# Kernel tuning notes

Measured on AMD Instinct MI355X. Metric: run time of the kernel, lower is better.

## Reference

```python
import jax, jax.numpy as jnp
import numpy as np

D_IN = 4096
D_OUT = 4096
EPS_NORM = 1e-6
EPS_Q = 1e-8


def _ternary_quantize(w):
    # per-output-channel absmean scale, then round/clamp to {-1,0,1}
    gamma = jnp.mean(jnp.abs(w), axis=-1)
    w_q = jnp.clip(jnp.round(w / (gamma[:, None] + EPS_Q)), -1.0, 1.0)
    return w_q, gamma


def setup_inputs() -> dict:
    key = jax.random.key(0)
    kx, kw = jax.random.split(key)
    x = jax.random.normal(kx, (2, 4096, D_IN), dtype=jnp.float32)
    # kaiming-uniform-like init then ternarize (mirrors torch __init__)
    bound = 1.0 / np.sqrt(D_IN)
    w_init = jax.random.uniform(kw, (D_OUT, D_IN), minval=-bound, maxval=bound, dtype=jnp.float32)
    w_q, gamma = _ternary_quantize(w_init)
    norm_weight = jnp.ones((D_IN,), dtype=jnp.float32)
    return {"x": x, "norm_weight": norm_weight, "w_q": w_q, "gamma": gamma}


def reference(x, norm_weight, w_q, gamma):
    # RMSNorm
    rms = jnp.sqrt(jnp.mean(x * x, axis=-1, keepdims=True) + EPS_NORM)
    xn = x / rms * norm_weight
    # ternary linear (dense fp32 GEMM, math identical to F.linear) + per-channel scale
    y = jnp.einsum('bsd,od->bso', xn, w_q) * gamma
    return y
```

## Files before the change

kernel.cpp:

```cpp
#include <hip/hip_runtime.h>
#include <hip/hip_bf16.h>
#include <stdint.h>

#define D_IN  4096
#define D_OUT 4096
#define MROWS 8192

using i32x4 = __attribute__((ext_vector_type(4))) int;

__global__ __launch_bounds__(256) void prep_kernel(
    const float* __restrict__ x, const float* __restrict__ nw,
    signed char* __restrict__ xq, float* __restrict__ srow,
    const float* __restrict__ wq, signed char* __restrict__ wb) {
  const int b = blockIdx.x;
  const int t = threadIdx.x;

  if (b < MROWS) {
    const float4* xr  = (const float4*)(x + (size_t)b * D_IN);
    const float4* nw4 = (const float4*)nw;

    float4 p[4];
    float ss = 0.f, mx = 0.f;
#pragma unroll
    for (int i = 0; i < 4; ++i) {
      const float4 v = xr[i * 256 + t];
      const float4 w = nw4[i * 256 + t];
      ss += v.x * v.x + v.y * v.y + v.z * v.z + v.w * v.w;
      p[i].x = v.x * w.x; p[i].y = v.y * w.y;
      p[i].z = v.z * w.z; p[i].w = v.w * w.w;
      mx = fmaxf(mx, fmaxf(fmaxf(fabsf(p[i].x), fabsf(p[i].y)),
                           fmaxf(fabsf(p[i].z), fabsf(p[i].w))));
    }
#pragma unroll
    for (int off = 32; off > 0; off >>= 1) {
      ss += __shfl_down(ss, off, 64);
      mx = fmaxf(mx, __shfl_down(mx, off, 64));
    }

    __shared__ float rs[4], rm[4];
    if ((t & 63) == 0) { rs[t >> 6] = ss; rm[t >> 6] = mx; }
    __syncthreads();
    const float scale =
        rsqrtf((rs[0] + rs[1] + rs[2] + rs[3]) * (1.0f / D_IN) + 1e-6f);
    const float rowmax = fmaxf(fmaxf(rm[0], rm[1]), fmaxf(rm[2], rm[3])) * scale;
    const float s   = fmaxf(rowmax, 1e-20f) * (1.0f / 127.0f);
    const float f   = scale / s;
    if (t == 0) srow[b] = s;

    int* out = (int*)(xq + (size_t)b * D_IN);
#pragma unroll
    for (int i = 0; i < 4; ++i) {
      const int q0 = (int)rintf(p[i].x * f);
      const int q1 = (int)rintf(p[i].y * f);
      const int q2 = (int)rintf(p[i].z * f);
      const int q3 = (int)rintf(p[i].w * f);
      out[i * 256 + t] =
          (q0 & 0xFF) | ((q1 & 0xFF) << 8) | ((q2 & 0xFF) << 16) | (q3 << 24);
    }
  } else {
    const int cb = b - MROWS;
    const float4* w4 = (const float4*)wq;
    int* o = (int*)wb;
#pragma unroll
    for (int i = 0; i < 4; ++i) {
      const int idx = cb * 1024 + i * 256 + t;
      const float4 v = w4[idx];
      const int q0 = (int)v.x, q1 = (int)v.y, q2 = (int)v.z, q3 = (int)v.w;
      o[idx] = (q0 & 0xFF) | ((q1 & 0xFF) << 8) | ((q2 & 0xFF) << 16) | (q3 << 24);
    }
  }
}

#define BM 128
#define BN 128
#define BKB 64

__global__ __launch_bounds__(256) void gemm_kernel(
    const signed char* __restrict__ A,
    const signed char* __restrict__ B,
    const float* __restrict__ srow,
    const float* __restrict__ gamma,
    float* __restrict__ C) {
  __shared__ __align__(16) signed char sA[BM * BKB];
  __shared__ __align__(16) signed char sB[BN * BKB];

  const int tid  = threadIdx.x;
  const int lane = tid & 63;
  const int wv   = tid >> 6;
  const int wm   = wv & 1;
  const int wn   = wv >> 1;
  const int bn   = blockIdx.x;
  const int bm   = blockIdx.y;

  i32x4 acc[4][4];
#pragma unroll
  for (int i = 0; i < 4; ++i)
#pragma unroll
    for (int j = 0; j < 4; ++j) acc[i][j] = (i32x4){0, 0, 0, 0};

  const size_t aBase = (size_t)(bm * BM) * D_IN;
  const size_t bBase = (size_t)(bn * BN) * D_IN;

  int r_[2], cc_[2];
#pragma unroll
  for (int i = 0; i < 2; ++i) {
    const int c = i * 256 + tid;
    r_[i]  = c >> 2;
    cc_[i] = ((c & 3) ^ ((r_[i] >> 1) & 3)) * 16;
  }

  for (int k0 = 0; k0 < D_IN; k0 += BKB) {
#pragma unroll
    for (int i = 0; i < 2; ++i) {
      __builtin_amdgcn_global_load_lds(
          (__attribute__((address_space(1))) void*)(A + aBase + (size_t)r_[i] * D_IN + k0 + cc_[i]),
          (__attribute__((address_space(3))) void*)&sA[(i * 256 + wv * 64) * 16],
          16, 0, 0);
    }
#pragma unroll
    for (int i = 0; i < 2; ++i) {
      __builtin_amdgcn_global_load_lds(
          (__attribute__((address_space(1))) void*)(B + bBase + (size_t)r_[i] * D_IN + k0 + cc_[i]),
          (__attribute__((address_space(3))) void*)&sB[(i * 256 + wv * 64) * 16],
          16, 0, 0);
    }
    __syncthreads();

    i32x4 af[4], bfr[4];
    const int m0 = wm * 64 + (lane & 15);
    const int n0 = wn * 64 + (lane & 15);
    const int kk = (((lane >> 4) ^ ((lane >> 1) & 3))) * 16;
#pragma unroll
    for (int i = 0; i < 4; ++i) af[i]  = *(const i32x4*)&sA[(m0 + i * 16) * BKB + kk];
#pragma unroll
    for (int j = 0; j < 4; ++j) bfr[j] = *(const i32x4*)&sB[(n0 + j * 16) * BKB + kk];

#pragma unroll
    for (int i = 0; i < 4; ++i)
#pragma unroll
      for (int j = 0; j < 4; ++j)
        acc[i][j] = __builtin_amdgcn_mfma_i32_16x16x64_i8(af[i], bfr[j], acc[i][j], 0, 0, 0);

    __syncthreads();
  }

  const int col0 = bn * BN + wn * 64 + (lane & 15);
  const int row0 = bm * BM + wm * 64 + ((lane >> 4) * 4);
  float sr[4][4];
#pragma unroll
  for (int i = 0; i < 4; ++i)
#pragma unroll
    for (int r = 0; r < 4; ++r) sr[i][r] = srow[row0 + i * 16 + r];

#pragma unroll
  for (int j = 0; j < 4; ++j) {
    const float g = gamma[col0 + j * 16];
#pragma unroll
    for (int i = 0; i < 4; ++i) {
      const int rb = row0 + i * 16;
#pragma unroll
      for (int r = 0; r < 4; ++r) {
        C[(size_t)(rb + r) * D_OUT + (col0 + j * 16)] =
            (float)acc[i][j][r] * sr[i][r] * g;
      }
    }
  }
}

extern "C" void kernel_launch(void* const* d_in, const int* in_sizes, int n_in,
                              void* d_out, int out_size, void* d_ws, size_t ws_size,
                              hipStream_t stream) {
  const float* x     = (const float*)d_in[0];
  const float* nw    = (const float*)d_in[1];
  const float* wq    = (const float*)d_in[2];
  const float* gamma = (const float*)d_in[3];
  float* y = (float*)d_out;

  signed char* xq = (signed char*)d_ws;
  signed char* wb = xq + (size_t)MROWS * D_IN;
  float* srow = (float*)(wb + (size_t)D_OUT * D_IN);

  prep_kernel<<<MROWS + 4096, 256, 0, stream>>>(x, nw, xq, srow, wq, wb);

  gemm_kernel<<<dim3(D_OUT / BN, MROWS / BM), 256, 0, stream>>>(xq, wb, srow, gamma, y);
}
```

Baseline: 428.8 us.

## Use 256x256 int8 GEMM tiles with a 4-stage LDS prefetch pipeline

Enlarges the GEMM tile to 256x256 with 512 threads (8 waves, each computing a 128x64 sub-tile). K slices are staged through a 4-deep ring of LDS buffers using direct global-to-LDS loads, with explicit vmcnt waits and barriers so loads overlap MFMA work. MFMA sections also raise wave priority. This aims to hide global load latency and halve per-output global traffic, at the cost of 128 KB of LDS and many more accumulator registers, which may limit occupancy.

```diff
diff --git a/kernel.cpp b/kernel.cpp
--- a/kernel.cpp
+++ b/kernel.cpp
@@ -71,101 +71,127 @@
   }
 }
 
-#define BM 128
-#define BN 128
+#define BM 256
+#define BN 256
 #define BKB 64
-
-__global__ __launch_bounds__(256) void gemm_kernel(
+#define NKT (D_IN / BKB)
+#define SLOT_BYTES (BM * BKB)
+
+#define WVM(n_) asm volatile("s_waitcnt vmcnt(" #n_ ")" ::: "memory")
+#define BAR()   __builtin_amdgcn_s_barrier()
+
+#define STAGE(t_, s_)                                                         \
+  do {                                                                        \
+    const int _k0 = (t_) * BKB;                                               \
+    _Pragma("unroll") for (int _i = 0; _i < 2; ++_i)                          \
+        __builtin_amdgcn_global_load_lds(                                     \
+            (__attribute__((address_space(1))) void*)(A + aOff[_i] + _k0),    \
+            (__attribute__((address_space(3))) void*)&sA[s_][ldsOff[_i]],     \
+            16, 0, 0);                                                        \
+    _Pragma("unroll") for (int _i = 0; _i < 2; ++_i)                          \
+        __builtin_amdgcn_global_load_lds(                                     \
+            (__attribute__((address_space(1))) void*)(B + bOff[_i] + _k0),    \
+            (__attribute__((address_space(3))) void*)&sB[s_][ldsOff[_i]],     \
+            16, 0, 0);                                                        \
+  } while (0)
+
+#define COMPUTE(s_)                                                           \
+  do {                                                                        \
+    i32x4 af[8], bfr[4];                                                      \
+    _Pragma("unroll") for (int _i = 0; _i < 8; ++_i)                          \
+        af[_i] = *(const i32x4*)&sA[s_][aoff + _i * (16 * BKB)];              \
+    _Pragma("unroll") for (int _j = 0; _j < 4; ++_j)                          \
+        bfr[_j] = *(const i32x4*)&sB[s_][boff + _j * (16 * BKB)];             \
+    __builtin_amdgcn_s_setprio(1);                                            \
+    _Pragma("unroll") for (int _i = 0; _i < 8; ++_i)                          \
+        _Pragma("unroll") for (int _j = 0; _j < 4; ++_j)                      \
+            acc[_i][_j] = __builtin_amdgcn_mfma_i32_16x16x64_i8(              \
+                af[_i], bfr[_j], acc[_i][_j], 0, 0, 0);                       \
+    __builtin_amdgcn_s_setprio(0);                                            \
+  } while (0)
+
+__global__ __launch_bounds__(512, 2) void gemm_kernel(
     const signed char* __restrict__ A,
     const signed char* __restrict__ B,
     const float* __restrict__ srow,
     const float* __restrict__ gamma,
     float* __restrict__ C) {
-  __shared__ __align__(16) signed char sA[BM * BKB];
-  __shared__ __align__(16) signed char sB[BN * BKB];
+  __shared__ __align__(16) signed char sA[4][SLOT_BYTES];
+  __shared__ __align__(16) signed char sB[4][SLOT_BYTES];
 
   const int tid  = threadIdx.x;
   const int lane = tid & 63;
   const int wv   = tid >> 6;
-  const int wm   = wv & 1;
-  const int wn   = wv >> 1;
+  const int wm   = wv >> 2;
+  const int wn   = wv & 3;
   const int bn   = blockIdx.x;
   const int bm   = blockIdx.y;
 
-  i32x4 acc[4][4];
-#pragma unroll
-  for (int i = 0; i < 4; ++i)
+  i32x4 acc[8][4];
+#pragma unroll
+  for (int i = 0; i < 8; ++i)
 #pragma unroll
     for (int j = 0; j < 4; ++j) acc[i][j] = (i32x4){0, 0, 0, 0};
 
-  const size_t aBase = (size_t)(bm * BM) * D_IN;
-  const size_t bBase = (size_t)(bn * BN) * D_IN;
-
-  int r_[2], cc_[2];
+  size_t aOff[2], bOff[2];
+  int ldsOff[2];
 #pragma unroll
   for (int i = 0; i < 2; ++i) {
-    const int c = i * 256 + tid;
-    r_[i]  = c >> 2;
-    cc_[i] = ((c & 3) ^ ((r_[i] >> 1) & 3)) * 16;
-  }
-
-  for (int k0 = 0; k0 < D_IN; k0 += BKB) {
-#pragma unroll
-    for (int i = 0; i < 2; ++i) {
-      __builtin_amdgcn_global_load_lds(
-          (__attribute__((address_space(1))) void*)(A + aBase + (size_t)r_[i] * D_IN + k0 + cc_[i]),
-          (__attribute__((address_space(3))) void*)&sA[(i * 256 + wv * 64) * 16],
-          16, 0, 0);
-    }
-#pragma unroll
-    for (int i = 0; i < 2; ++i) {
-      __builtin_amdgcn_global_load_lds(
-          (__attribute__((address_space(1))) void*)(B + bBase + (size_t)r_[i] * D_IN + k0 + cc_[i]),
-          (__attribute__((address_space(3))) void*)&sB[(i * 256 + wv * 64) * 16],
-          16, 0, 0);
-    }
-    __syncthreads();
-
-    i32x4 af[4], bfr[4];
-    const int m0 = wm * 64 + (lane & 15);
-    const int n0 = wn * 64 + (lane & 15);
-    const int kk = (((lane >> 4) ^ ((lane >> 1) & 3))) * 16;
-#pragma unroll
-    for (int i = 0; i < 4; ++i) af[i]  = *(const i32x4*)&sA[(m0 + i * 16) * BKB + kk];
-#pragma unroll
-    for (int j = 0; j < 4; ++j) bfr[j] = *(const i32x4*)&sB[(n0 + j * 16) * BKB + kk];
-
-#pragma unroll
-    for (int i = 0; i < 4; ++i)
-#pragma unroll
-      for (int j = 0; j < 4; ++j)
-        acc[i][j] = __builtin_amdgcn_mfma_i32_16x16x64_i8(af[i], bfr[j], acc[i][j], 0, 0, 0);
-
-    __syncthreads();
-  }
+    const int c  = i * 512 + tid;
+    const int r  = c >> 2;
+    const int cc = ((c & 3) ^ ((r >> 1) & 3)) * 16;
+    aOff[i] = (size_t)(bm * BM + r) * D_IN + cc;
+    bOff[i] = (size_t)(bn * BN + r) * D_IN + cc;
+    ldsOff[i] = (i * 512 + wv * 64) * 16;
+  }
+
+  const int kk   = (((lane >> 4) ^ ((lane >> 1) & 3))) * 16;
+  const int aoff = (wm * 128 + (lane & 15)) * BKB + kk;
+  const int boff = (wn * 64  + (lane & 15)) * BKB + kk;
+
+  STAGE(0, 0);
+  STAGE(1, 1);
+  STAGE(2, 2);
+  WVM(8);
+  BAR();
+
+#pragma unroll 1
+  for (int t4 = 0; t4 < NKT - 4; t4 += 4) {
+    STAGE(t4 + 3, 3); COMPUTE(0); WVM(8); BAR();
+    STAGE(t4 + 4, 0); COMPUTE(1); WVM(8); BAR();
+    STAGE(t4 + 5, 1); COMPUTE(2); WVM(8); BAR();
+    STAGE(t4 + 6, 2); COMPUTE(3); WVM(8); BAR();
+  }
+  STAGE(NKT - 1, 3); COMPUTE(0); WVM(8); BAR();
+  COMPUTE(1); WVM(4); BAR();
+  COMPUTE(2); WVM(0); BAR();
+  COMPUTE(3);
 
   const int col0 = bn * BN + wn * 64 + (lane & 15);
-  const int row0 = bm * BM + wm * 64 + ((lane >> 4) * 4);
-  float sr[4][4];
-#pragma unroll
-  for (int i = 0; i < 4; ++i)
-#pragma unroll
-    for (int r = 0; r < 4; ++r) sr[i][r] = srow[row0 + i * 16 + r];
-
-#pragma unroll
-  for (int j = 0; j < 4; ++j) {
-    const float g = gamma[col0 + j * 16];
-#pragma unroll
-    for (int i = 0; i < 4; ++i) {
-      const int rb = row0 + i * 16;
-#pragma unroll
-      for (int r = 0; r < 4; ++r) {
-        C[(size_t)(rb + r) * D_OUT + (col0 + j * 16)] =
-            (float)acc[i][j][r] * sr[i][r] * g;
+  const int row0 = bm * BM + wm * 128 + ((lane >> 4) * 4);
+  float g[4];
+#pragma unroll
+  for (int j = 0; j < 4; ++j) g[j] = gamma[col0 + j * 16];
+
+#pragma unroll
+  for (int i = 0; i < 8; ++i) {
+#pragma unroll
+    for (int r = 0; r < 4; ++r) {
+      const int row = row0 + i * 16 + r;
+      const float sr = srow[row];
+#pragma unroll
+      for (int j = 0; j < 4; ++j) {
+        C[(size_t)row * D_OUT + col0 + j * 16] =
+            (float)acc[i][j][r] * sr * g[j];
       }
     }
   }
 }
+
+#undef STAGE
+#undef COMPUTE
+#undef WVM
+#undef BAR
 
 extern "C" void kernel_launch(void* const* d_in, const int* in_sizes, int n_in,
                               void* d_out, int out_size, void* d_ws, size_t ws_size,
@@ -182,5 +208,5 @@
 
   prep_kernel<<<MROWS + 4096, 256, 0, stream>>>(x, nw, xq, srow, wq, wb);
 
-  gemm_kernel<<<dim3(D_OUT / BN, MROWS / BM), 256, 0, stream>>>(xq, wb, srow, gamma, y);
+  gemm_kernel<<<dim3(D_OUT / BN, MROWS / BM), 512, 0, stream>>>(xq, wb, srow, gamma, y);
 }
```

Measured after the change: 388.0 us. 1.11x faster.
